# Kernel optimization log

Measured on AMD Instinct MI355X. Metric: run time of the kernel, lower is better.

The kernel has to match this reference:

```python
import jax, jax.numpy as jnp
import numpy as np

DEGREE = 7

def setup_inputs() -> dict:
    key = jax.random.key(0)
    k1, k2 = jax.random.split(key)
    input_dims, output_dims = 1024, 1024
    x = jax.random.normal(k1, (8192, input_dims), dtype=jnp.float32)
    std = 1.0 / (input_dims * (DEGREE + 1))
    lucas_coeffs = std * jax.random.normal(k2, (input_dims, output_dims, DEGREE + 1), dtype=jnp.float32)
    return {"x": x, "lucas_coeffs": lucas_coeffs}

def reference(x, lucas_coeffs):
    input_dims = lucas_coeffs.shape[0]
    x = x.reshape(-1, input_dims)
    x = jnp.tanh(x)
    # Lucas polynomial recurrence: L0=2, L1=x, L_i = x*L_{i-1} + L_{i-2}
    basis = [jnp.full_like(x, 2.0)]
    if DEGREE > 0:
        basis.append(x)
    for i in range(2, DEGREE + 1):
        basis.append(x * basis[-1] + basis[-2])
    lucas = jnp.stack(basis, axis=-1)  # [b, i, d]
    y = jnp.einsum('bid,iod->bo', lucas, lucas_coeffs)
    return y
```

## Files before the change

### kernel.cpp

```cpp
#include <hip/hip_runtime.h>
#include <hip/hip_bf16.h>


typedef __attribute__((ext_vector_type(8)))  short  short8;
typedef __attribute__((ext_vector_type(4)))  unsigned short ushort4v;
typedef __attribute__((ext_vector_type(8)))  unsigned short ushort8;
typedef __attribute__((ext_vector_type(4)))  float  float4v;
typedef __attribute__((ext_vector_type(4)))  unsigned int uint4v;

#define M_DIM 8192
#define I_DIM 1024
#define O_DIM 1024
#define K_DIM 8192
#define BM 64
#define BN 128
#define BK 64
#define NSTEP (K_DIM / BK)

__device__ __forceinline__ unsigned short f2bf(float f) {
    unsigned int u = __float_as_uint(f);
    u += 0x7FFFu + ((u >> 16) & 1u);
    return (unsigned short)(u >> 16);
}

__global__ __launch_bounds__(256) void prep_t_kernel(const float* __restrict__ x,
                                                     unsigned short* __restrict__ T) {
    int idx = (blockIdx.x * 256 + threadIdx.x) * 4;
    float4v v = *(const float4v*)(x + idx);
    ushort4v o;
    o[0] = f2bf(tanhf(v[0]));
    o[1] = f2bf(tanhf(v[1]));
    o[2] = f2bf(tanhf(v[2]));
    o[3] = f2bf(tanhf(v[3]));
    *(ushort4v*)(T + idx) = o;
}

__global__ __launch_bounds__(256) void prep_b_kernel(const float* __restrict__ c,
                                                     unsigned short* __restrict__ Bt) {
    int idx = blockIdx.x * 256 + threadIdx.x;
    int i = idx >> 10;
    int o = idx & 1023;
    const float* src = c + (size_t)i * 8192 + o * 8;
    float4v lo = *(const float4v*)(src);
    float4v hi = *(const float4v*)(src + 4);
    ushort8 v;
    v[0] = f2bf(lo[0]); v[1] = f2bf(lo[1]); v[2] = f2bf(lo[2]); v[3] = f2bf(lo[3]);
    v[4] = f2bf(hi[0]); v[5] = f2bf(hi[1]); v[6] = f2bf(hi[2]); v[7] = f2bf(hi[3]);
    *(ushort8*)(Bt + (size_t)o * K_DIM + i * 8) = v;
}

__device__ __forceinline__ short8 lucas_frag(unsigned int tb) {
    const float t = __uint_as_float(tb << 16);
    const float L2v = fmaf(t, t, 2.0f);
    const float L3v = fmaf(t, L2v, t);
    const float L4v = fmaf(t, L3v, L2v);
    const float L5v = fmaf(t, L4v, L3v);
    const float L6v = fmaf(t, L5v, L4v);
    const float L7v = fmaf(t, L6v, L5v);
    const unsigned int u2 = __float_as_uint(L2v) + 0x8000u;
    const unsigned int u3 = __float_as_uint(L3v) + 0x8000u;
    const unsigned int u4 = __float_as_uint(L4v) + 0x8000u;
    const unsigned int u5 = __float_as_uint(L5v) + 0x8000u;
    const unsigned int u6 = __float_as_uint(L6v) + 0x8000u;
    const unsigned int u7 = __float_as_uint(L7v) + 0x8000u;
    union { uint4v u; short8 s; } r;
    r.u[0] = 0x4000u | (tb << 16);
    r.u[1] = __builtin_amdgcn_perm(u3, u2, 0x07060302);
    r.u[2] = __builtin_amdgcn_perm(u5, u4, 0x07060302);
    r.u[3] = __builtin_amdgcn_perm(u7, u6, 0x07060302);
    return r.s;
}

__global__ __launch_bounds__(256, 4) void gemm_kernel(const unsigned short* __restrict__ T,
                                                      const unsigned short* __restrict__ Bt,
                                                      float* __restrict__ out) {
    __shared__ unsigned short Bs[2][BN * BK];
    __shared__ unsigned short Ts[2][BM * 8];

    const int tid  = threadIdx.x;
    const int lane = tid & 63;
    const int wave = tid >> 6;
    const int m0 = blockIdx.x * BM;
    const int n0 = blockIdx.y * BN;

    const int wm0  = (wave >> 1) * 32;
    const int wn0  = (wave & 1) * 64;
    const int l16  = lane & 15;
    const int quad = lane >> 4;

    const int srow   = lane >> 3;
    const int il     = lane & 7;
    const int gchunk = il ^ srow;

    float4v acc[2][4];
    const float4v zero = {0.f, 0.f, 0.f, 0.f};
    #pragma unroll
    for (int a = 0; a < 2; ++a)
        #pragma unroll
        for (int b = 0; b < 4; ++b) acc[a][b] = zero;

    #pragma unroll
    for (int r = 0; r < 4; ++r) {
        const int rowb = r * 32 + wave * 8;
        const unsigned short* gB = Bt + (size_t)(n0 + rowb + srow) * K_DIM + gchunk * 8;
        __builtin_amdgcn_global_load_lds(
            (const __attribute__((address_space(1))) unsigned int*)gB,
            (__attribute__((address_space(3))) unsigned int*)&Bs[0][rowb * BK], 16, 0, 0);
    }
    if (wave == 0) {
        const unsigned short* gT = T + (size_t)(m0 + lane) * I_DIM;
        __builtin_amdgcn_global_load_lds(
            (const __attribute__((address_space(1))) unsigned int*)gT,
            (__attribute__((address_space(3))) unsigned int*)&Ts[0][0], 16, 0, 0);
    }
    __syncthreads();

    int cur = 0;
    for (int s = 0; s < NSTEP; ++s) {
        const int nxt = cur ^ 1;

        if (s + 1 < NSTEP) {
            const int kt = (s + 1) * BK;
            #pragma unroll
            for (int r = 0; r < 4; ++r) {
                const int rowb = r * 32 + wave * 8;
                const unsigned short* gB = Bt + (size_t)(n0 + rowb + srow) * K_DIM + kt + gchunk * 8;
                __builtin_amdgcn_global_load_lds(
                    (const __attribute__((address_space(1))) unsigned int*)gB,
                    (__attribute__((address_space(3))) unsigned int*)&Bs[nxt][rowb * BK], 16, 0, 0);
            }
            if (wave == 0) {
                const unsigned short* gT = T + (size_t)(m0 + lane) * I_DIM + kt / 8;
                __builtin_amdgcn_global_load_lds(
                    (const __attribute__((address_space(1))) unsigned int*)gT,
                    (__attribute__((address_space(3))) unsigned int*)&Ts[nxt][0], 16, 0, 0);
            }
        }

        unsigned int tb[2][2];
        #pragma unroll
        for (int tt = 0; tt < 2; ++tt)
            #pragma unroll
            for (int k2 = 0; k2 < 2; ++k2)
                tb[tt][k2] = Ts[cur][(wm0 + tt * 16 + l16) * 8 + (k2 * 4 + quad)];

        #pragma unroll
        for (int k2 = 0; k2 < 2; ++k2) {
            short8 af[2];
            af[0] = lucas_frag(tb[0][k2]);
            af[1] = lucas_frag(tb[1][k2]);
            short8 bfr[4];
            #pragma unroll
            for (int tn = 0; tn < 4; ++tn) {
                const int brow = wn0 + tn * 16 + l16;
                bfr[tn] = *(const short8*)&Bs[cur][brow * BK + (((k2 * 4 + quad) ^ (l16 & 7)) * 8)];
            }
            #pragma unroll
            for (int tt = 0; tt < 2; ++tt)
                #pragma unroll
                for (int tn = 0; tn < 4; ++tn)
                    acc[tt][tn] = __builtin_amdgcn_mfma_f32_16x16x32_bf16(
                        af[tt], bfr[tn], acc[tt][tn], 0, 0, 0);
        }

        __syncthreads();
        cur = nxt;
    }

    #pragma unroll
    for (int tt = 0; tt < 2; ++tt) {
        #pragma unroll
        for (int tn = 0; tn < 4; ++tn) {
            const int col = n0 + wn0 + tn * 16 + l16;
            #pragma unroll
            for (int r = 0; r < 4; ++r) {
                const int row = m0 + wm0 + tt * 16 + quad * 4 + r;
                out[(size_t)row * O_DIM + col] = acc[tt][tn][r];
            }
        }
    }
}

__global__ __launch_bounds__(256) void naive_kernel(const float* __restrict__ x,
                                                    const float* __restrict__ c,
                                                    float* __restrict__ out) {
    int idx = blockIdx.x * 256 + threadIdx.x;
    int b = idx >> 10;
    int o = idx & 1023;
    const float* xb = x + (size_t)b * I_DIM;
    float acc = 0.f;
    for (int i = 0; i < I_DIM; ++i) {
        float t = tanhf(xb[i]);
        float L[8];
        L[0] = 2.0f; L[1] = t;
        #pragma unroll
        for (int d = 2; d < 8; ++d) L[d] = t * L[d - 1] + L[d - 2];
        const float* cc = c + (size_t)i * 8192 + o * 8;
        #pragma unroll
        for (int d = 0; d < 8; ++d) acc += L[d] * cc[d];
    }
    out[idx] = acc;
}

extern "C" void kernel_launch(void* const* d_in, const int* in_sizes, int n_in,
                              void* d_out, int out_size, void* d_ws, size_t ws_size,
                              hipStream_t stream) {
    const float* x      = (const float*)d_in[0];
    const float* coeffs = (const float*)d_in[1];
    float* out = (float*)d_out;

    const size_t btBytes = (size_t)O_DIM * K_DIM * sizeof(unsigned short);
    const size_t tBytes  = (size_t)M_DIM * I_DIM * sizeof(unsigned short);

    if (ws_size >= btBytes + tBytes) {
        unsigned short* Bt = (unsigned short*)d_ws;
        unsigned short* T  = (unsigned short*)((char*)d_ws + btBytes);

        prep_b_kernel<<<(I_DIM * O_DIM) / 256, 256, 0, stream>>>(coeffs, Bt);
        prep_t_kernel<<<(M_DIM * I_DIM) / (4 * 256), 256, 0, stream>>>(x, T);

        dim3 grid(M_DIM / BM, O_DIM / BN);
        gemm_kernel<<<grid, 256, 0, stream>>>(T, Bt, out);
    } else {
        naive_kernel<<<(M_DIM * O_DIM) / 256, 256, 0, stream>>>(x, coeffs, out);
    }
}
```

Measured before the change: 268.5 us.

## Load GEMM operands directly to registers, drop LDS, widen tile, merge prep kernels

The GEMM kernel no longer stages B and T tiles through shared memory. Each wave loads its own bf16 B fragments and tanh values straight from global memory into registers, double-buffered in registers, and each block now covers a 64x256 output tile with a 64x64 tile per wave. This removes LDS traffic and the per-step barriers, and the two prep kernels are fused into one launch. In exchange, waves that share a block no longer share B data, so global and L2 traffic rise. Register pressure also grows, and occupancy is capped at 2 blocks per CU.

```diff
diff --git a/kernel.cpp b/kernel.cpp
--- a/kernel.cpp
+++ b/kernel.cpp
@@ -13,7 +13,7 @@
 #define O_DIM 1024
 #define K_DIM 8192
 #define BM 64
-#define BN 128
+#define BN 256
 #define BK 64
 #define NSTEP (K_DIM / BK)
 
@@ -23,30 +23,32 @@
     return (unsigned short)(u >> 16);
 }
 
-__global__ __launch_bounds__(256) void prep_t_kernel(const float* __restrict__ x,
-                                                     unsigned short* __restrict__ T) {
-    int idx = (blockIdx.x * 256 + threadIdx.x) * 4;
-    float4v v = *(const float4v*)(x + idx);
-    ushort4v o;
-    o[0] = f2bf(tanhf(v[0]));
-    o[1] = f2bf(tanhf(v[1]));
-    o[2] = f2bf(tanhf(v[2]));
-    o[3] = f2bf(tanhf(v[3]));
-    *(ushort4v*)(T + idx) = o;
-}
-
-__global__ __launch_bounds__(256) void prep_b_kernel(const float* __restrict__ c,
-                                                     unsigned short* __restrict__ Bt) {
-    int idx = blockIdx.x * 256 + threadIdx.x;
-    int i = idx >> 10;
-    int o = idx & 1023;
-    const float* src = c + (size_t)i * 8192 + o * 8;
-    float4v lo = *(const float4v*)(src);
-    float4v hi = *(const float4v*)(src + 4);
-    ushort8 v;
-    v[0] = f2bf(lo[0]); v[1] = f2bf(lo[1]); v[2] = f2bf(lo[2]); v[3] = f2bf(lo[3]);
-    v[4] = f2bf(hi[0]); v[5] = f2bf(hi[1]); v[6] = f2bf(hi[2]); v[7] = f2bf(hi[3]);
-    *(ushort8*)(Bt + (size_t)o * K_DIM + i * 8) = v;
+__global__ __launch_bounds__(256) void prep_kernel(const float* __restrict__ x,
+                                                   const float* __restrict__ c,
+                                                   unsigned short* __restrict__ T,
+                                                   unsigned short* __restrict__ Bt) {
+    int bid = blockIdx.x;
+    if (bid < (M_DIM * I_DIM) / (4 * 256)) {
+        int idx = (bid * 256 + threadIdx.x) * 4;
+        float4v v = *(const float4v*)(x + idx);
+        ushort4v o;
+        o[0] = f2bf(tanhf(v[0]));
+        o[1] = f2bf(tanhf(v[1]));
+        o[2] = f2bf(tanhf(v[2]));
+        o[3] = f2bf(tanhf(v[3]));
+        *(ushort4v*)(T + idx) = o;
+    } else {
+        int idx = (bid - (M_DIM * I_DIM) / (4 * 256)) * 256 + threadIdx.x;
+        int i = idx >> 10;
+        int o = idx & 1023;
+        const float* src = c + (size_t)i * 8192 + o * 8;
+        float4v lo = *(const float4v*)(src);
+        float4v hi = *(const float4v*)(src + 4);
+        ushort8 v;
+        v[0] = f2bf(lo[0]); v[1] = f2bf(lo[1]); v[2] = f2bf(lo[2]); v[3] = f2bf(lo[3]);
+        v[4] = f2bf(hi[0]); v[5] = f2bf(hi[1]); v[6] = f2bf(hi[2]); v[7] = f2bf(hi[3]);
+        *(ushort8*)(Bt + (size_t)o * K_DIM + i * 8) = v;
+    }
 }
 
 __device__ __forceinline__ short8 lucas_frag(unsigned int tb) {
@@ -71,110 +73,84 @@
     return r.s;
 }
 
-__global__ __launch_bounds__(256, 4) void gemm_kernel(const unsigned short* __restrict__ T,
+__global__ __launch_bounds__(256, 2) void gemm_kernel(const unsigned short* __restrict__ T,
                                                       const unsigned short* __restrict__ Bt,
                                                       float* __restrict__ out) {
-    __shared__ unsigned short Bs[2][BN * BK];
-    __shared__ unsigned short Ts[2][BM * 8];
-
     const int tid  = threadIdx.x;
     const int lane = tid & 63;
     const int wave = tid >> 6;
-    const int m0 = blockIdx.x * BM;
-    const int n0 = blockIdx.y * BN;
-
-    const int wm0  = (wave >> 1) * 32;
-    const int wn0  = (wave & 1) * 64;
+    const int n0w = blockIdx.x * BN + wave * 64;
+    const int m0  = blockIdx.y * BM;
+
     const int l16  = lane & 15;
     const int quad = lane >> 4;
 
-    const int srow   = lane >> 3;
-    const int il     = lane & 7;
-    const int gchunk = il ^ srow;
-
-    float4v acc[2][4];
+    int boff[8], toff[8];
+    #pragma unroll
+    for (int tn = 0; tn < 4; ++tn)
+        #pragma unroll
+        for (int k2 = 0; k2 < 2; ++k2)
+            boff[tn * 2 + k2] = (n0w + tn * 16 + l16) * K_DIM + k2 * 32 + quad * 8;
+    #pragma unroll
+    for (int tt = 0; tt < 4; ++tt)
+        #pragma unroll
+        for (int k2 = 0; k2 < 2; ++k2)
+            toff[tt * 2 + k2] = (m0 + tt * 16 + l16) * I_DIM + k2 * 4 + quad;
+
+    float4v acc[4][4];
     const float4v zero = {0.f, 0.f, 0.f, 0.f};
     #pragma unroll
-    for (int a = 0; a < 2; ++a)
+    for (int a = 0; a < 4; ++a)
         #pragma unroll
         for (int b = 0; b < 4; ++b) acc[a][b] = zero;
 
-    #pragma unroll
-    for (int r = 0; r < 4; ++r) {
-        const int rowb = r * 32 + wave * 8;
-        const unsigned short* gB = Bt + (size_t)(n0 + rowb + srow) * K_DIM + gchunk * 8;
-        __builtin_amdgcn_global_load_lds(
-            (const __attribute__((address_space(1))) unsigned int*)gB,
-            (__attribute__((address_space(3))) unsigned int*)&Bs[0][rowb * BK], 16, 0, 0);
-    }
-    if (wave == 0) {
-        const unsigned short* gT = T + (size_t)(m0 + lane) * I_DIM;
-        __builtin_amdgcn_global_load_lds(
-            (const __attribute__((address_space(1))) unsigned int*)gT,
-            (__attribute__((address_space(3))) unsigned int*)&Ts[0][0], 16, 0, 0);
-    }
-    __syncthreads();
-
-    int cur = 0;
+    short8 bcur[8];
+    unsigned short tcur[8];
+    #pragma unroll
+    for (int j = 0; j < 8; ++j) {
+        bcur[j] = *(const short8*)(Bt + boff[j]);
+        tcur[j] = T[toff[j]];
+        boff[j] += BK;
+        toff[j] += 8;
+    }
+
     for (int s = 0; s < NSTEP; ++s) {
-        const int nxt = cur ^ 1;
-
+        short8 bnxt[8];
+        unsigned short tnxt[8];
         if (s + 1 < NSTEP) {
-            const int kt = (s + 1) * BK;
             #pragma unroll
-            for (int r = 0; r < 4; ++r) {
-                const int rowb = r * 32 + wave * 8;
-                const unsigned short* gB = Bt + (size_t)(n0 + rowb + srow) * K_DIM + kt + gchunk * 8;
-                __builtin_amdgcn_global_load_lds(
-                    (const __attribute__((address_space(1))) unsigned int*)gB,
-                    (__attribute__((address_space(3))) unsigned int*)&Bs[nxt][rowb * BK], 16, 0, 0);
-            }
-            if (wave == 0) {
-                const unsigned short* gT = T + (size_t)(m0 + lane) * I_DIM + kt / 8;
-                __builtin_amdgcn_global_load_lds(
-                    (const __attribute__((address_space(1))) unsigned int*)gT,
-                    (__attribute__((address_space(3))) unsigned int*)&Ts[nxt][0], 16, 0, 0);
+            for (int j = 0; j < 8; ++j) {
+                bnxt[j] = *(const short8*)(Bt + boff[j]);
+                tnxt[j] = T[toff[j]];
+                boff[j] += BK;
+                toff[j] += 8;
             }
         }
 
-        unsigned int tb[2][2];
-        #pragma unroll
-        for (int tt = 0; tt < 2; ++tt)
+        #pragma unroll
+        for (int k2 = 0; k2 < 2; ++k2) {
             #pragma unroll
-            for (int k2 = 0; k2 < 2; ++k2)
-                tb[tt][k2] = Ts[cur][(wm0 + tt * 16 + l16) * 8 + (k2 * 4 + quad)];
-
-        #pragma unroll
-        for (int k2 = 0; k2 < 2; ++k2) {
-            short8 af[2];
-            af[0] = lucas_frag(tb[0][k2]);
-            af[1] = lucas_frag(tb[1][k2]);
-            short8 bfr[4];
-            #pragma unroll
-            for (int tn = 0; tn < 4; ++tn) {
-                const int brow = wn0 + tn * 16 + l16;
-                bfr[tn] = *(const short8*)&Bs[cur][brow * BK + (((k2 * 4 + quad) ^ (l16 & 7)) * 8)];
-            }
-            #pragma unroll
-            for (int tt = 0; tt < 2; ++tt)
+            for (int tt = 0; tt < 4; ++tt) {
+                const short8 af = lucas_frag(tcur[tt * 2 + k2]);
                 #pragma unroll
                 for (int tn = 0; tn < 4; ++tn)
                     acc[tt][tn] = __builtin_amdgcn_mfma_f32_16x16x32_bf16(
-                        af[tt], bfr[tn], acc[tt][tn], 0, 0, 0);
+                        af, bcur[tn * 2 + k2], acc[tt][tn], 0, 0, 0);
+            }
         }
 
-        __syncthreads();
-        cur = nxt;
-    }
-
-    #pragma unroll
-    for (int tt = 0; tt < 2; ++tt) {
+        #pragma unroll
+        for (int j = 0; j < 8; ++j) { bcur[j] = bnxt[j]; tcur[j] = tnxt[j]; }
+    }
+
+    #pragma unroll
+    for (int tt = 0; tt < 4; ++tt) {
         #pragma unroll
         for (int tn = 0; tn < 4; ++tn) {
-            const int col = n0 + wn0 + tn * 16 + l16;
+            const int col = n0w + tn * 16 + l16;
             #pragma unroll
             for (int r = 0; r < 4; ++r) {
-                const int row = m0 + wm0 + tt * 16 + quad * 4 + r;
+                const int row = m0 + tt * 16 + quad * 4 + r;
                 out[(size_t)row * O_DIM + col] = acc[tt][tn][r];
             }
         }
@@ -216,10 +192,11 @@
         unsigned short* Bt = (unsigned short*)d_ws;
         unsigned short* T  = (unsigned short*)((char*)d_ws + btBytes);
 
-        prep_b_kernel<<<(I_DIM * O_DIM) / 256, 256, 0, stream>>>(coeffs, Bt);
-        prep_t_kernel<<<(M_DIM * I_DIM) / (4 * 256), 256, 0, stream>>>(x, T);
-
-        dim3 grid(M_DIM / BM, O_DIM / BN);
+        const int tBlocks = (M_DIM * I_DIM) / (4 * 256);
+        const int bBlocks = (I_DIM * O_DIM) / 256;
+        prep_kernel<<<tBlocks + bBlocks, 256, 0, stream>>>(x, coeffs, T, Bt);
+
+        dim3 grid(O_DIM / BN, M_DIM / BM);
         gemm_kernel<<<grid, 256, 0, stream>>>(T, Bt, out);
     } else {
         naive_kernel<<<(M_DIM * O_DIM) / 256, 256, 0, stream>>>(x, coeffs, out);
```

New measurement: 556.5 us. 107% more time.
